# Kernel optimization log

Hardware: AMD Instinct MI355X
Metric: run time of the kernel (lower is better)

Reference implementation:

```python
import jax, jax.numpy as jnp
import numpy as np

BINS = 32
SIGMA = 5.0
DELTA = 1.0


def _soft_cdf(img):
    # img: (B, C, D, H, W) in [0, 1]
    B, C, D, H, W = img.shape
    x = (img * (BINS - 1)).reshape(B * C, 1, -1)           # (BC, 1, N)
    centers = jnp.arange(BINS, dtype=jnp.float32)[None, :, None]  # (1, bins, 1)
    # soft bin membership via difference of sigmoids, summed over voxels
    soft_bins = (jax.nn.sigmoid((x - centers + DELTA / 2) * SIGMA)
                 - jax.nn.sigmoid((x - centers - DELTA / 2) * SIGMA))  # (BC, bins, N)
    hist = soft_bins.sum(axis=2)                            # (BC, bins)
    # F.normalize(p=1, dim=1)
    hist = hist / jnp.maximum(jnp.sum(jnp.abs(hist), axis=1, keepdims=True), 1e-12)
    return jnp.cumsum(hist, axis=1)                         # CDF, (BC, bins)


def setup_inputs() -> dict:
    key = jax.random.key(0)
    k1, k2 = jax.random.split(key)
    shape = (2, 1, 64, 128, 128)
    dst = jax.random.uniform(k1, shape, dtype=jnp.float32)
    ref = jax.random.uniform(k2, shape, dtype=jnp.float32)
    return {"dst": dst, "ref": ref}


def reference(dst, ref):
    B, C, D, H, W = dst.shape
    cdf_dst = _soft_cdf(dst)                                # (BC, bins)
    cdf_ref = _soft_cdf(ref)                                # (BC, bins)
    # CDF matching: for each src bin, nearest ref bin by |cdf difference|
    dist = jnp.abs(cdf_dst[:, :, None] - cdf_ref[:, None, :])  # (BC, bins, bins)
    tables = jnp.argmin(dist, axis=2).astype(jnp.float32)      # (BC, bins)
    # soft lookup: Gaussian-softmax weights over bin indices
    dst_flat = dst.reshape(B * C, -1)[:, :, None] * (BINS - 1)    # (BC, N, 1)
    indices = jnp.arange(BINS, dtype=jnp.float32)[None, None, :]  # (1, 1, bins)
    weights = jax.nn.softmax(-(dst_flat - indices) ** 2 / (2 * SIGMA ** 2), axis=-1)
    matched = jnp.einsum('bnk,bk->bn', weights, tables)     # (BC, N)
    return matched.reshape(B, C, D, H, W) / (BINS - 1)
```

## Files before the change

kernel.cpp:

```cpp
#include <hip/hip_runtime.h>
#include <math.h>

#define NVOX  1048576
#define NSLC  4
#define MFINE 2048
#define BINS  32
#define PB    64
#define HIST_BLOCKS  (NSLC * PB)
#define APPLY_BLOCKS 512
#define NLUT  2048


__global__ __launch_bounds__(512) void hist_kernel(const float4* __restrict__ dst4,
                                                   const float4* __restrict__ ref4,
                                                   float* __restrict__ partial) {
    __shared__ unsigned int h[MFINE];
    const int t  = threadIdx.x;
    const int b  = blockIdx.x;
    const int s  = b >> 6;
    const int ib = b & 63;

    for (int i = t; i < MFINE; i += 512) h[i] = 0;
    __syncthreads();

    const float4* src = (s < 2) ? (dst4 + s * (NVOX / 4))
                                : (ref4 + (s - 2) * (NVOX / 4));
    const int base = ib * 4096;

    float4 v[8];
    #pragma unroll
    for (int j = 0; j < 8; ++j) v[j] = src[base + j * 512 + t];

    #pragma unroll
    for (int j = 0; j < 8; ++j) {
        int m0 = min(max((int)(v[j].x * (float)MFINE), 0), MFINE - 1);
        int m1 = min(max((int)(v[j].y * (float)MFINE), 0), MFINE - 1);
        int m2 = min(max((int)(v[j].z * (float)MFINE), 0), MFINE - 1);
        int m3 = min(max((int)(v[j].w * (float)MFINE), 0), MFINE - 1);
        atomicAdd(&h[m0], 1u);
        atomicAdd(&h[m1], 1u);
        atomicAdd(&h[m2], 1u);
        atomicAdd(&h[m3], 1u);
    }
    __syncthreads();

    const int c = t >> 4;
    const int j = t & 15;
    const float fc = (float)c;
    const float DY = 31.0f / (float)MFINE;
    const float c1 = 12.1825190f;
    const float c2 = 12.3467369f;

    int i0 = (int)ceilf((fc - 4.5f) * ((float)MFINE / 31.0f) - 0.5f);
    int i1 = (int)floorf((fc + 4.5f) * ((float)MFINE / 31.0f) - 0.5f);
    if (i0 < 0) i0 = 0;
    if (i1 > MFINE - 1) i1 = MFINE - 1;

    const float Kstep = __expf(80.0f * DY);
    float d0 = fmaf((float)(i0 + j), DY, 0.5f * DY - fc);
    float E  = __expf(5.0f * d0);

    float acc = 0.f;
    for (int i = i0 + j; i <= i1; i += 16) {
        float cnt = (float)h[i];
        float den = fmaf(E, c2, fmaf(E, E, 1.0f));
        acc = fmaf(cnt * E, c1 * __builtin_amdgcn_rcpf(den), acc);
        E *= Kstep;
    }
    acc += __shfl_xor(acc, 1, 64);
    acc += __shfl_xor(acc, 2, 64);
    acc += __shfl_xor(acc, 4, 64);
    acc += __shfl_xor(acc, 8, 64);
    if (j == 0) partial[(s * BINS + c) * PB + ib] = acc;
}

__global__ __launch_bounds__(256) void apply_kernel(const float4* __restrict__ dst4,
                                                    const float* __restrict__ partial,
                                                    float4* __restrict__ out4) {
    __shared__ float slut[NLUT];
    __shared__ float softS[64];
    __shared__ float cdfS[64];
    __shared__ float gS[BINS];
    __shared__ float gtS[BINS];
    const int t  = threadIdx.x;
    const int b  = blockIdx.x;
    const int s  = b >> 8;
    const int ib = b & 255;

    const int base = s * (NVOX / 4) + ib * 1024;
    float4 v[4];
    #pragma unroll
    for (int j = 0; j < 4; ++j) v[j] = dst4[base + j * 256 + t];

    {
        const int r = t >> 2, j = t & 3;
        const int grow = (r < 32) ? (s * BINS + r) : ((2 + s) * BINS + (r - 32));
        const float4* prow = (const float4*)(partial + grow * PB);
        float4 a4 = make_float4(0.f, 0.f, 0.f, 0.f);
        #pragma unroll
        for (int m = 0; m < 4; ++m) {
            float4 p = prow[j + 4 * m];
            a4.x += p.x; a4.y += p.y; a4.z += p.z; a4.w += p.w;
        }
        float acc = (a4.x + a4.y) + (a4.z + a4.w);
        acc += __shfl_xor(acc, 1, 64);
        acc += __shfl_xor(acc, 2, 64);
        if (j == 0) softS[r] = acc;
    }
    __syncthreads();

    if (t < 64) {
        float v2 = softS[t];
        #pragma unroll
        for (int off = 1; off < BINS; off <<= 1) {
            float w = __shfl_up(v2, off, 32);
            if ((t & 31) >= off) v2 += w;
        }
        float total = __shfl(v2, 31, 32);
        cdfS[t] = v2 / fmaxf(total, 1e-12f);
    }
    __syncthreads();

    if (t < 32) {
        float v2 = cdfS[t];
        int best = 0;
        float bd = fabsf(v2 - cdfS[32]);
        #pragma unroll
        for (int k = 1; k < BINS; ++k) {
            float dk = fabsf(v2 - cdfS[32 + k]);
            if (dk < bd) { bd = dk; best = k; }
        }
        float g = __expf(-(float)(t * t) * (1.0f / 50.0f));
        gtS[t] = g * (float)best;
        gS[t]  = g;
    }
    __syncthreads();

    for (int e = t; e < NLUT; e += 256) {
        float y = (float)e * (31.0f / (float)(NLUT - 1));
        float r = __expf(y * (1.0f / 25.0f));
        float u = 1.f, num = 0.f, den = 0.f;
        #pragma unroll
        for (int k = 0; k < BINS; ++k) {
            num = fmaf(u, gtS[k], num);
            den = fmaf(u, gS[k], den);
            u *= r;
        }
        slut[e] = num * __builtin_amdgcn_rcpf(den) * (1.0f / 31.0f);
    }
    __syncthreads();

    float* x = (float*)v;
    #pragma unroll
    for (int i = 0; i < 16; ++i) {
        float p = x[i] * (float)(NLUT - 1);
        p = fminf(fmaxf(p, 0.f), (float)(NLUT - 1) - 1.0f);
        int   ix = (int)p;
        float fr = p - (float)ix;
        float lo = slut[ix], hi = slut[ix + 1];
        x[i] = fmaf(fr, hi - lo, lo);
    }
    #pragma unroll
    for (int j = 0; j < 4; ++j) out4[base + j * 256 + t] = v[j];
}

extern "C" void kernel_launch(void* const* d_in, const int* in_sizes, int n_in,
                              void* d_out, int out_size, void* d_ws, size_t ws_size,
                              hipStream_t stream) {
    const float4* dst4 = (const float4*)d_in[0];
    const float4* ref4 = (const float4*)d_in[1];
    float4* out4 = (float4*)d_out;
    float* partial = (float*)d_ws;

    hipLaunchKernelGGL(hist_kernel,  dim3(HIST_BLOCKS),  dim3(512), 0, stream,
                       dst4, ref4, partial);
    hipLaunchKernelGGL(apply_kernel, dim3(APPLY_BLOCKS), dim3(256), 0, stream,
                       dst4, partial, out4);
}
```

Baseline: 76.60 us.

## Fuse histogram and apply kernels into one cooperative launch with grid sync

Merges the histogram kernel and the apply kernel into a single cooperative kernel of 256 blocks that synchronises across the whole grid between phases. Each block preloads its apply-phase dst slice into registers before the histogram work, so the second read of dst overlaps with the first phase and the second kernel launch goes away. The cost is a grid-wide barrier, higher register and shared-memory use per block (histogram plus LUT), and the requirement that all blocks be co-resident.

Result: slower. 109.0 us (+42.3%).

```diff
diff --git a/kernel.cpp b/kernel.cpp
--- a/kernel.cpp
+++ b/kernel.cpp
@@ -1,35 +1,49 @@
 #include <hip/hip_runtime.h>
+#include <hip/hip_cooperative_groups.h>
 #include <math.h>
 
+namespace cg = cooperative_groups;
+
 #define NVOX  1048576
-#define NSLC  4
 #define MFINE 2048
 #define BINS  32
 #define PB    64
-#define HIST_BLOCKS  (NSLC * PB)
-#define APPLY_BLOCKS 512
+#define GRID  256
 #define NLUT  2048
 
 
-__global__ __launch_bounds__(512) void hist_kernel(const float4* __restrict__ dst4,
-                                                   const float4* __restrict__ ref4,
-                                                   float* __restrict__ partial) {
+__global__ __launch_bounds__(512) void fused_kernel(const float4* __restrict__ dst4,
+                                                    const float4* __restrict__ ref4,
+                                                    float* __restrict__ partial,
+                                                    float4* __restrict__ out4) {
     __shared__ unsigned int h[MFINE];
+    __shared__ float slut[NLUT];
+    __shared__ float softS[64];
+    __shared__ float cdfS[64];
+    __shared__ float gS[BINS];
+    __shared__ float gtS[BINS];
+
     const int t  = threadIdx.x;
     const int b  = blockIdx.x;
     const int s  = b >> 6;
     const int ib = b & 63;
+    const int as_ = b >> 7;
+    const int ia  = b & 127;
+
+    const int abase = as_ * (NVOX / 4) + ia * 2048;
+    float4 a[4];
+    #pragma unroll
+    for (int j = 0; j < 4; ++j) a[j] = dst4[abase + j * 512 + t];
+
+    const float4* src = (s < 2) ? (dst4 + s * (NVOX / 4))
+                                : (ref4 + (s - 2) * (NVOX / 4));
+    const int hbase = ib * 4096;
+    float4 v[8];
+    #pragma unroll
+    for (int j = 0; j < 8; ++j) v[j] = src[hbase + j * 512 + t];
 
     for (int i = t; i < MFINE; i += 512) h[i] = 0;
     __syncthreads();
-
-    const float4* src = (s < 2) ? (dst4 + s * (NVOX / 4))
-                                : (ref4 + (s - 2) * (NVOX / 4));
-    const int base = ib * 4096;
-
-    float4 v[8];
-    #pragma unroll
-    for (int j = 0; j < 8; ++j) v[j] = src[base + j * 512 + t];
 
     #pragma unroll
     for (int j = 0; j < 8; ++j) {
@@ -44,67 +58,53 @@
     }
     __syncthreads();
 
-    const int c = t >> 4;
-    const int j = t & 15;
-    const float fc = (float)c;
-    const float DY = 31.0f / (float)MFINE;
-    const float c1 = 12.1825190f;
-    const float c2 = 12.3467369f;
+    {
+        const int c = t >> 4;
+        const int j = t & 15;
+        const float fc = (float)c;
+        const float DY = 31.0f / (float)MFINE;
+        const float c1 = 12.1825190f;
+        const float c2 = 12.3467369f;
 
-    int i0 = (int)ceilf((fc - 4.5f) * ((float)MFINE / 31.0f) - 0.5f);
-    int i1 = (int)floorf((fc + 4.5f) * ((float)MFINE / 31.0f) - 0.5f);
-    if (i0 < 0) i0 = 0;
-    if (i1 > MFINE - 1) i1 = MFINE - 1;
+        int i0 = (int)ceilf((fc - 4.5f) * ((float)MFINE / 31.0f) - 0.5f);
+        int i1 = (int)floorf((fc + 4.5f) * ((float)MFINE / 31.0f) - 0.5f);
+        if (i0 < 0) i0 = 0;
+        if (i1 > MFINE - 1) i1 = MFINE - 1;
 
-    const float Kstep = __expf(80.0f * DY);
-    float d0 = fmaf((float)(i0 + j), DY, 0.5f * DY - fc);
-    float E  = __expf(5.0f * d0);
+        const float Kstep = __expf(80.0f * DY);
+        float d0 = fmaf((float)(i0 + j), DY, 0.5f * DY - fc);
+        float E  = __expf(5.0f * d0);
 
-    float acc = 0.f;
-    for (int i = i0 + j; i <= i1; i += 16) {
-        float cnt = (float)h[i];
-        float den = fmaf(E, c2, fmaf(E, E, 1.0f));
-        acc = fmaf(cnt * E, c1 * __builtin_amdgcn_rcpf(den), acc);
-        E *= Kstep;
+        float acc = 0.f;
+        for (int i = i0 + j; i <= i1; i += 16) {
+            float cnt = (float)h[i];
+            float den = fmaf(E, c2, fmaf(E, E, 1.0f));
+            acc = fmaf(cnt * E, c1 * __builtin_amdgcn_rcpf(den), acc);
+            E *= Kstep;
+        }
+        acc += __shfl_xor(acc, 1, 64);
+        acc += __shfl_xor(acc, 2, 64);
+        acc += __shfl_xor(acc, 4, 64);
+        acc += __shfl_xor(acc, 8, 64);
+        if (j == 0) partial[(s * BINS + c) * PB + ib] = acc;
     }
-    acc += __shfl_xor(acc, 1, 64);
-    acc += __shfl_xor(acc, 2, 64);
-    acc += __shfl_xor(acc, 4, 64);
-    acc += __shfl_xor(acc, 8, 64);
-    if (j == 0) partial[(s * BINS + c) * PB + ib] = acc;
-}
 
-__global__ __launch_bounds__(256) void apply_kernel(const float4* __restrict__ dst4,
-                                                    const float* __restrict__ partial,
-                                                    float4* __restrict__ out4) {
-    __shared__ float slut[NLUT];
-    __shared__ float softS[64];
-    __shared__ float cdfS[64];
-    __shared__ float gS[BINS];
-    __shared__ float gtS[BINS];
-    const int t  = threadIdx.x;
-    const int b  = blockIdx.x;
-    const int s  = b >> 8;
-    const int ib = b & 255;
-
-    const int base = s * (NVOX / 4) + ib * 1024;
-    float4 v[4];
-    #pragma unroll
-    for (int j = 0; j < 4; ++j) v[j] = dst4[base + j * 256 + t];
+    cg::this_grid().sync();
 
     {
-        const int r = t >> 2, j = t & 3;
-        const int grow = (r < 32) ? (s * BINS + r) : ((2 + s) * BINS + (r - 32));
+        const int r = t >> 3, j = t & 7;
+        const int grow = (r < 32) ? (as_ * BINS + r) : ((2 + as_) * BINS + (r - 32));
         const float4* prow = (const float4*)(partial + grow * PB);
         float4 a4 = make_float4(0.f, 0.f, 0.f, 0.f);
         #pragma unroll
-        for (int m = 0; m < 4; ++m) {
-            float4 p = prow[j + 4 * m];
+        for (int m = 0; m < 2; ++m) {
+            float4 p = prow[j + 8 * m];
             a4.x += p.x; a4.y += p.y; a4.z += p.z; a4.w += p.w;
         }
         float acc = (a4.x + a4.y) + (a4.z + a4.w);
         acc += __shfl_xor(acc, 1, 64);
         acc += __shfl_xor(acc, 2, 64);
+        acc += __shfl_xor(acc, 4, 64);
         if (j == 0) softS[r] = acc;
     }
     __syncthreads();
@@ -136,7 +136,7 @@
     }
     __syncthreads();
 
-    for (int e = t; e < NLUT; e += 256) {
+    for (int e = t; e < NLUT; e += 512) {
         float y = (float)e * (31.0f / (float)(NLUT - 1));
         float r = __expf(y * (1.0f / 25.0f));
         float u = 1.f, num = 0.f, den = 0.f;
@@ -150,7 +150,7 @@
     }
     __syncthreads();
 
-    float* x = (float*)v;
+    float* x = (float*)a;
     #pragma unroll
     for (int i = 0; i < 16; ++i) {
         float p = x[i] * (float)(NLUT - 1);
@@ -161,7 +161,7 @@
         x[i] = fmaf(fr, hi - lo, lo);
     }
     #pragma unroll
-    for (int j = 0; j < 4; ++j) out4[base + j * 256 + t] = v[j];
+    for (int j = 0; j < 4; ++j) out4[abase + j * 512 + t] = a[j];
 }
 
 extern "C" void kernel_launch(void* const* d_in, const int* in_sizes, int n_in,
@@ -172,8 +172,7 @@
     float4* out4 = (float4*)d_out;
     float* partial = (float*)d_ws;
 
-    hipLaunchKernelGGL(hist_kernel,  dim3(HIST_BLOCKS),  dim3(512), 0, stream,
-                       dst4, ref4, partial);
-    hipLaunchKernelGGL(apply_kernel, dim3(APPLY_BLOCKS), dim3(256), 0, stream,
-                       dst4, partial, out4);
+    void* args[] = { (void*)&dst4, (void*)&ref4, (void*)&partial, (void*)&out4 };
+    hipLaunchCooperativeKernel((const void*)fused_kernel, dim3(GRID), dim3(512),
+                               args, 0, stream);
 }
```
